# Kernel tuning notes

Measured on AMD Instinct MI355X. Metric: run time of the kernel, lower is better.

## Reference

```python
import jax, jax.numpy as jnp
import numpy as np

N_OSC = 128
N_AUDIO = 32768
NYQUIST = 22050 / 2.0
BASE_FREQ = 40.0 / NYQUIST
MAX_FREQ = 9000.0 / NYQUIST
FREQ_RANGE = MAX_FREQ - BASE_FREQ


def _interp_linear(a, out_size):
    # torch F.interpolate(mode='linear', align_corners=False) along last axis
    T = a.shape[-1]
    scale = T / out_size
    pos = (jnp.arange(out_size, dtype=a.dtype) + 0.5) * scale - 0.5
    pos = jnp.clip(pos, 0.0, T - 1)
    i0 = jnp.floor(pos).astype(jnp.int32)
    i1 = jnp.minimum(i0 + 1, T - 1)
    w = pos - i0.astype(a.dtype)
    return a[..., i0] * (1.0 - w) + a[..., i1] * w


def setup_inputs() -> dict:
    key = jax.random.key(0)
    k1, k2, k3, k4 = jax.random.split(key, 4)
    batch, channels, time = 4, 128, 128
    x = jax.random.normal(k1, (batch, channels, time), dtype=jnp.float32)
    # Conv1d(input_channels, n_osc*2, kernel=1) -> weight [2*n_osc, C], bias [2*n_osc]
    W = jax.random.normal(k2, (2 * N_OSC, channels), dtype=jnp.float32) * (1.0 / np.sqrt(channels))
    b = jax.random.normal(k3, (2 * N_OSC,), dtype=jnp.float32) * 0.01
    baselines = jax.random.uniform(k4, (N_OSC, 2), dtype=jnp.float32, minval=0.0, maxval=0.1)
    return {"x": x, "W": W, "b": b, "baselines": baselines}


def reference(x, W, b, baselines):
    batch, channels, time = x.shape
    # 1x1 conv = per-timestep matmul: [B, 2*n_osc, T]
    h = jnp.einsum('bct,oc->bot', x, W) + b[None, :, None]
    h = h.reshape(batch, N_OSC, 2, time)
    h = h * 0.01 + baselines[None, :, :, None]
    r = h[:, :, 0, :]
    i = h[:, :, 1, :]
    amp = jnp.sqrt(r * r + i * i)          # torch.norm over dim=2
    freq = jnp.arctan2(i, r) / np.pi       # torch.angle / pi
    freq = freq ** 2
    amp = amp ** 2
    amp = BASE_FREQ + amp * FREQ_RANGE
    amp = _interp_linear(amp, N_AUDIO)     # [B, n_osc, N_AUDIO]
    freq = _interp_linear(freq, N_AUDIO)
    phase = jnp.cumsum(freq * np.pi, axis=-1)
    osc = jnp.sin(phase) * amp
    osc = jnp.sum(osc, axis=1, keepdims=True)  # [B, 1, N_AUDIO]
    return osc
```

## Files before the change

kernel.cpp:

```cpp
#include <hip/hip_runtime.h>
#include <math.h>

#define BATCH 4
#define CH 128
#define NOSC 128
#define TK 128
#define NAUD 32768
#define NVS 129


__global__ __launch_bounds__(512) void osc1_kernel(
    const float* __restrict__ x, const float* __restrict__ W,
    const float* __restrict__ bvec, const float* __restrict__ baselines,
    float* __restrict__ seg)
{
    const int blk = blockIdx.x;
    const int b = blk >> 7, o = blk & 127;
    const int tid = threadIdx.x;
    const int k = tid & 127;
    const int c0 = __builtin_amdgcn_readfirstlane(tid >> 7) * 32;

    const float* __restrict__ Wr = W + (2*o)*CH;
    const float* __restrict__ Wi = Wr + CH;
    const float* xb = x + b*CH*TK + k;

    float re = 0.f, im = 0.f;
    {
        float xv[32];
        #pragma unroll
        for (int u = 0; u < 32; ++u) xv[u] = xb[(c0+u)*TK];
        #pragma unroll
        for (int u = 0; u < 32; ++u) { re = fmaf(xv[u], Wr[c0+u], re); im = fmaf(xv[u], Wi[c0+u], im); }
    }

    __shared__ float sRe[512], sIm[512];
    sRe[tid] = re; sIm[tid] = im;
    __syncthreads();

    __shared__ float fsh[TK], ash[TK];
    __shared__ double wtot;
    float fr = 0.f, amp = 0.f;
    if (tid < 128) {
        float rr = sRe[tid] + sRe[tid+128] + sRe[tid+256] + sRe[tid+384] + bvec[2*o];
        float ii = sIm[tid] + sIm[tid+128] + sIm[tid+256] + sIm[tid+384] + bvec[2*o+1];
        rr = fmaf(rr, 0.01f, baselines[2*o]);
        ii = fmaf(ii, 0.01f, baselines[2*o+1]);
        const float BASEF  = 40.0f/11025.0f;
        const float RANGEF = 8960.0f/11025.0f;
        amp = fmaf(fmaf(rr, rr, ii*ii), RANGEF, BASEF);
        float th = atan2f(ii, rr) * (1.0f/3.14159265358979323846f);
        fr = th*th;
        fsh[k] = fr; ash[k] = amp;
    }
    __syncthreads();

    double ev = 0.0;
    if (tid < 128) {
        ev = (k == 0) ? 128.0*(double)fr
                      : 128.0*((double)fsh[k-1] + (double)fr);
        const int lane = tid & 63;
        #pragma unroll
        for (int d = 1; d < 64; d <<= 1) {
            double up = __shfl_up(ev, d);
            if (lane >= d) ev += up;
        }
        if (tid == 63) wtot = ev;
    }
    __syncthreads();
    if (tid < 128) {
        if (tid >= 64) ev += wtot;
        double xrev = ev * 0.5;
        float cRev = (float)(xrev - floor(xrev));

        float* base = seg + ((size_t)(b*NVS)*NOSC + o)*8;
        const int vs = k + 1;
        float f0h = 0.5f*fr;
        float dfh = (k <= 126) ? 0.5f*(fsh[k+1] - fr) : 0.0f;
        float da  = (k <= 126) ? (ash[k+1] - amp) : 0.0f;
        float* p = base + (size_t)vs*NOSC*8;
        *(float4*)p = make_float4(f0h, dfh, cRev, amp);
        p[4] = da;
        if (k == 0) {
            *(float4*)base = make_float4(f0h, 0.0f, 0.0f, amp);
            base[4] = 0.0f;
        }
    }
}

__global__ __launch_bounds__(512) void osc2_kernel(
    const float* __restrict__ seg, float* __restrict__ out)
{
    const int blk = blockIdx.x;
    const int b   = blk >> 7;
    const int z   = blk & 127;
    const int tid = threadIdx.x;
    const int s   = tid & 31;
    const int g   = tid >> 5;

    __shared__ float4 tupA[256];
    __shared__ float4 tupB[256];
    __shared__ float  red[16][256];

    const float4* srcA = (const float4*)(seg + ((size_t)(b*NVS) + (z == 0 ? 0 : z))*NOSC*8);
    if (z == 0) {
        const float4* srcB = (const float4*)(seg + ((size_t)(b*NVS) + 128)*NOSC*8);
        if (tid < 256) tupA[tid]       = srcA[tid];
        else           tupB[tid - 256] = srcB[tid - 256];
    } else {
        if (tid < 256) tupA[tid] = srcA[tid];
    }
    __syncthreads();

    float acc[8] = {0.f,0.f,0.f,0.f,0.f,0.f,0.f,0.f};
    const float* bpA = (const float*)&tupA[g*16];
    const float* bpB = (const float*)&tupB[g*16];

    if (z != 0) {
        float jp1_[8], jsq_[8], w_[8];
        #pragma unroll
        for (int m = 0; m < 8; ++m) {
            float jp1 = (float)(32*m + s + 1);
            jp1_[m] = jp1;
            jsq_[m] = jp1*jp1*(1.0f/512.0f);
            w_[m]   = (2.0f*jp1 - 1.0f)*(1.0f/512.0f);
        }
        #pragma unroll
        for (int i = 0; i < 8; ++i) {
            float4 v = *(const float4*)(bpA + i*8);
            float da = bpA[i*8 + 4];
            #pragma unroll
            for (int m = 0; m < 8; ++m) {
                float rev = fmaf(v.y, jsq_[m], fmaf(jp1_[m], v.x, v.z));
                float fr_, sn;
                asm("v_fract_f32 %0, %1" : "=v"(fr_) : "v"(rev));
                asm("v_sin_f32 %0, %1"   : "=v"(sn)  : "v"(fr_));
                acc[m] = fmaf(fmaf(da, w_[m], v.w), sn, acc[m]);
            }
        }
    } else {
        float jp1_[4], jsq_[4], w_[4];
        #pragma unroll
        for (int m = 0; m < 4; ++m) {
            float jp1 = (float)(32*m + s + 1);
            jp1_[m] = jp1;
            jsq_[m] = jp1*jp1*(1.0f/512.0f);
            w_[m]   = (2.0f*jp1 - 1.0f)*(1.0f/512.0f);
        }
        #pragma unroll
        for (int i = 0; i < 8; ++i) {
            float4 vA = *(const float4*)(bpA + i*8);
            float daA = bpA[i*8 + 4];
            float4 vB = *(const float4*)(bpB + i*8);
            float daB = bpB[i*8 + 4];
            #pragma unroll
            for (int m = 0; m < 4; ++m) {
                float fr_, sn;
                float revA = fmaf(vA.y, jsq_[m], fmaf(jp1_[m], vA.x, vA.z));
                asm("v_fract_f32 %0, %1" : "=v"(fr_) : "v"(revA));
                asm("v_sin_f32 %0, %1"   : "=v"(sn)  : "v"(fr_));
                acc[m] = fmaf(fmaf(daA, w_[m], vA.w), sn, acc[m]);
                float revB = fmaf(vB.y, jsq_[m], fmaf(jp1_[m], vB.x, vB.z));
                asm("v_fract_f32 %0, %1" : "=v"(fr_) : "v"(revB));
                asm("v_sin_f32 %0, %1"   : "=v"(sn)  : "v"(fr_));
                acc[4+m] = fmaf(fmaf(daB, w_[m], vB.w), sn, acc[4+m]);
            }
        }
    }

    #pragma unroll
    for (int m = 0; m < 8; ++m)
        red[g][s + 32*m] = acc[m];
    __syncthreads();

    if (tid < 256) {
        float v = 0.f;
        #pragma unroll
        for (int gg = 0; gg < 16; ++gg) v += red[gg][tid];
        int t = (z != 0) ? ((2*z - 1)*128 + tid)
                         : ((tid < 128) ? tid : (NAUD - 256 + tid));
        out[b*NAUD + t] = v;
    }
}

extern "C" void kernel_launch(void* const* d_in, const int* in_sizes, int n_in,
                              void* d_out, int out_size, void* d_ws, size_t ws_size,
                              hipStream_t stream)
{
    const float* x         = (const float*)d_in[0];
    const float* W         = (const float*)d_in[1];
    const float* bvec      = (const float*)d_in[2];
    const float* baselines = (const float*)d_in[3];
    float* out = (float*)d_out;
    float* seg = (float*)d_ws;

    osc1_kernel<<<BATCH*NOSC, 512, 0, stream>>>(x, W, bvec, baselines, seg);
    osc2_kernel<<<BATCH*128, 512, 0, stream>>>(seg, out);
}
```

Before: 15.32 us.

## Remap osc2 to wave-per-oscillator-group and read segments directly from global

Result: slower. 15.92 us (+3.9%).

```diff
diff --git a/kernel.cpp b/kernel.cpp
--- a/kernel.cpp
+++ b/kernel.cpp
@@ -94,88 +94,75 @@
     const int b   = blk >> 7;
     const int z   = blk & 127;
     const int tid = threadIdx.x;
-    const int s   = tid & 31;
-    const int g   = tid >> 5;
+    const int l   = tid & 63;
+    const int w   = __builtin_amdgcn_readfirstlane(tid >> 6);
 
-    __shared__ float4 tupA[256];
-    __shared__ float4 tupB[256];
-    __shared__ float  red[16][256];
+    __shared__ float red[8][256];
 
-    const float4* srcA = (const float4*)(seg + ((size_t)(b*NVS) + (z == 0 ? 0 : z))*NOSC*8);
-    if (z == 0) {
-        const float4* srcB = (const float4*)(seg + ((size_t)(b*NVS) + 128)*NOSC*8);
-        if (tid < 256) tupA[tid]       = srcA[tid];
-        else           tupB[tid - 256] = srcB[tid - 256];
-    } else {
-        if (tid < 256) tupA[tid] = srcA[tid];
-    }
-    __syncthreads();
-
-    float acc[8] = {0.f,0.f,0.f,0.f,0.f,0.f,0.f,0.f};
-    const float* bpA = (const float*)&tupA[g*16];
-    const float* bpB = (const float*)&tupB[g*16];
+    float acc[4] = {0.f, 0.f, 0.f, 0.f};
 
     if (z != 0) {
-        float jp1_[8], jsq_[8], w_[8];
+        const float* __restrict__ p = seg + ((size_t)(b*NVS + z)*NOSC + w*16)*8;
+        float jp1_[4], jsq_[4], ww_[4];
         #pragma unroll
-        for (int m = 0; m < 8; ++m) {
-            float jp1 = (float)(32*m + s + 1);
+        for (int m = 0; m < 4; ++m) {
+            float jp1 = (float)(64*m + l + 1);
             jp1_[m] = jp1;
             jsq_[m] = jp1*jp1*(1.0f/512.0f);
-            w_[m]   = (2.0f*jp1 - 1.0f)*(1.0f/512.0f);
+            ww_[m]  = (2.0f*jp1 - 1.0f)*(1.0f/512.0f);
         }
         #pragma unroll
-        for (int i = 0; i < 8; ++i) {
-            float4 v = *(const float4*)(bpA + i*8);
-            float da = bpA[i*8 + 4];
+        for (int i = 0; i < 16; ++i) {
+            const float f0h = p[i*8+0], dfh = p[i*8+1], cR = p[i*8+2];
+            const float a0  = p[i*8+3], da  = p[i*8+4];
             #pragma unroll
-            for (int m = 0; m < 8; ++m) {
-                float rev = fmaf(v.y, jsq_[m], fmaf(jp1_[m], v.x, v.z));
+            for (int m = 0; m < 4; ++m) {
+                float rev = fmaf(dfh, jsq_[m], fmaf(jp1_[m], f0h, cR));
                 float fr_, sn;
                 asm("v_fract_f32 %0, %1" : "=v"(fr_) : "v"(rev));
                 asm("v_sin_f32 %0, %1"   : "=v"(sn)  : "v"(fr_));
-                acc[m] = fmaf(fmaf(da, w_[m], v.w), sn, acc[m]);
+                acc[m] = fmaf(fmaf(da, ww_[m], a0), sn, acc[m]);
             }
         }
     } else {
-        float jp1_[4], jsq_[4], w_[4];
+        const float* __restrict__ pH = seg + ((size_t)(b*NVS +   0)*NOSC + w*16)*8;
+        const float* __restrict__ pT = seg + ((size_t)(b*NVS + 128)*NOSC + w*16)*8;
+        float jp1_[2], jsq_[2], ww_[2];
         #pragma unroll
-        for (int m = 0; m < 4; ++m) {
-            float jp1 = (float)(32*m + s + 1);
+        for (int m = 0; m < 2; ++m) {
+            float jp1 = (float)(64*m + l + 1);
             jp1_[m] = jp1;
             jsq_[m] = jp1*jp1*(1.0f/512.0f);
-            w_[m]   = (2.0f*jp1 - 1.0f)*(1.0f/512.0f);
+            ww_[m]  = (2.0f*jp1 - 1.0f)*(1.0f/512.0f);
         }
         #pragma unroll
-        for (int i = 0; i < 8; ++i) {
-            float4 vA = *(const float4*)(bpA + i*8);
-            float daA = bpA[i*8 + 4];
-            float4 vB = *(const float4*)(bpB + i*8);
-            float daB = bpB[i*8 + 4];
+        for (int i = 0; i < 16; ++i) {
+            const float f0hH = pH[i*8+0], cRH = pH[i*8+2], a0H = pH[i*8+3];
+            const float f0hT = pT[i*8+0], cRT = pT[i*8+2], a0T = pT[i*8+3];
             #pragma unroll
-            for (int m = 0; m < 4; ++m) {
+            for (int m = 0; m < 2; ++m) {
                 float fr_, sn;
-                float revA = fmaf(vA.y, jsq_[m], fmaf(jp1_[m], vA.x, vA.z));
-                asm("v_fract_f32 %0, %1" : "=v"(fr_) : "v"(revA));
+                float revH = fmaf(jp1_[m], f0hH, cRH);
+                asm("v_fract_f32 %0, %1" : "=v"(fr_) : "v"(revH));
                 asm("v_sin_f32 %0, %1"   : "=v"(sn)  : "v"(fr_));
-                acc[m] = fmaf(fmaf(daA, w_[m], vA.w), sn, acc[m]);
-                float revB = fmaf(vB.y, jsq_[m], fmaf(jp1_[m], vB.x, vB.z));
-                asm("v_fract_f32 %0, %1" : "=v"(fr_) : "v"(revB));
+                acc[m] = fmaf(a0H, sn, acc[m]);
+                float revT = fmaf(jp1_[m], f0hT, cRT);
+                asm("v_fract_f32 %0, %1" : "=v"(fr_) : "v"(revT));
                 asm("v_sin_f32 %0, %1"   : "=v"(sn)  : "v"(fr_));
-                acc[4+m] = fmaf(fmaf(daB, w_[m], vB.w), sn, acc[4+m]);
+                acc[2+m] = fmaf(a0T, sn, acc[2+m]);
             }
         }
     }
 
     #pragma unroll
-    for (int m = 0; m < 8; ++m)
-        red[g][s + 32*m] = acc[m];
+    for (int m = 0; m < 4; ++m)
+        red[w][64*m + l] = acc[m];
     __syncthreads();
 
     if (tid < 256) {
         float v = 0.f;
         #pragma unroll
-        for (int gg = 0; gg < 16; ++gg) v += red[gg][tid];
+        for (int gg = 0; gg < 8; ++gg) v += red[gg][tid];
         int t = (z != 0) ? ((2*z - 1)*128 + tid)
                          : ((tid < 128) ? tid : (NAUD - 256 + tid));
         out[b*NAUD + t] = v;
```
